# Performance work log

Hardware: AMD Instinct MI355X
Metric: run time of the kernel (lower is better)

The kernel has to match this reference:

```python
import jax, jax.numpy as jnp
import numpy as np

N_NODES = 50000
N_EDGES = 800000
N_GRAPHS = 256
D_IN = 128
D_HID = 128


def setup_inputs() -> dict:
    key = jax.random.key(0)
    ks = jax.random.split(key, 10)
    x = jax.random.normal(ks[0], (N_NODES, D_IN), dtype=jnp.float32)
    edge_index = jax.random.randint(ks[1], (2, N_EDGES), 0, N_NODES, dtype=jnp.int64)
    batch = jnp.sort(jax.random.randint(ks[2], (N_NODES,), 0, N_GRAPHS, dtype=jnp.int64))
    def lin(k, din, dout):
        s = 1.0 / np.sqrt(din)
        return jax.random.uniform(k, (din, dout), jnp.float32, -s, s)
    W1 = lin(ks[3], D_IN, D_HID); b1 = jnp.zeros((D_HID,), jnp.float32)
    W2 = lin(ks[4], D_HID, D_HID); b2 = jnp.zeros((D_HID,), jnp.float32)
    W3 = lin(ks[5], D_HID, D_HID); b3 = jnp.zeros((D_HID,), jnp.float32)
    return {"x": x, "edge_index": edge_index, "batch": batch,
            "W1": W1, "b1": b1, "W2": W2, "b2": b2, "W3": W3, "b3": b3}


def _gcn_norm(edge_index, num_nodes):
    # PyG gcn_norm with add_self_loops=True, edge_weight=1
    loops = jnp.arange(num_nodes, dtype=edge_index.dtype)
    src = jnp.concatenate([edge_index[0], loops])
    dst = jnp.concatenate([edge_index[1], loops])
    ones = jnp.ones(src.shape[0], jnp.float32)
    deg = jax.ops.segment_sum(ones, dst, num_segments=num_nodes)
    dinv = jnp.where(deg > 0, jax.lax.rsqrt(deg), 0.0)
    norm = dinv[src] * dinv[dst]
    return src, dst, norm


def _gcn_conv(x, src, dst, norm, W, b, num_nodes):
    h = x @ W                              # [N, dout] transform first
    msg = h[src] * norm[:, None]           # gather + scale  [E+N, dout]
    agg = jax.ops.segment_sum(msg, dst, num_segments=num_nodes)
    return agg + b


def reference(x, edge_index, batch, W1, b1, W2, b2, W3, b3):
    n = x.shape[0]
    src, dst, norm = _gcn_norm(edge_index, n)
    h = jax.nn.relu(_gcn_conv(x, src, dst, norm, W1, b1, n))
    h = jax.nn.relu(_gcn_conv(h, src, dst, norm, W2, b2, n))
    h = _gcn_conv(h, src, dst, norm, W3, b3, n)
    # global_mean_pool over batch ids
    sums = jax.ops.segment_sum(h, batch, num_segments=N_GRAPHS)
    cnts = jax.ops.segment_sum(jnp.ones((n,), jnp.float32), batch, num_segments=N_GRAPHS)
    return sums / jnp.maximum(cnts, 1.0)[:, None]
```

## Files before the change

### kernel.cpp

```cpp
#include <hip/hip_runtime.h>

#define N_NODES 50000
#define N_PAD   50048
#define N_EDGES 800000
#define N_GRAPHS 256
#define D 128
#define CAP 64
#define GEMM_GRID (N_PAD / 64)

typedef short bf16x8 __attribute__((ext_vector_type(8)));
typedef float f32x4  __attribute__((ext_vector_type(4)));

__device__ inline unsigned short f2bf(float f) {
    unsigned u = __float_as_uint(f);
    u += 0x7FFF + ((u >> 16) & 1);
    return (unsigned short)(u >> 16);
}
__device__ inline float bf2f(unsigned short b) { return __uint_as_float((unsigned)b << 16); }

__global__ __launch_bounds__(256) void k_pack(const float* __restrict__ W1, const float* __restrict__ W2,
                                              const float* __restrict__ W3, unsigned short* __restrict__ Wp) {
    int idx = blockIdx.x * 256 + threadIdx.x;
    if (idx >= 3 * D * D) return;
    int L = idx >> 14, rem = idx & 16383;
    int k = rem >> 7, n = rem & 127;
    const float* W = (L == 0) ? W1 : (L == 1) ? W2 : W3;
    float w = W[k * D + n];
    int kt = k >> 5, kg = (k >> 3) & 3, i = k & 7;
    int nt = n >> 4, ln = kg * 16 + (n & 15);
    size_t dst = (size_t)L * 32768 + ((size_t)(kt * 8 + nt) * 64 + ln) * 8 + i;
    unsigned short hi = f2bf(w);
    Wp[dst]         = hi;
    Wp[dst + 16384] = f2bf(w - bf2f(hi));
}

__global__ __launch_bounds__(256) void k_fill(const int* __restrict__ ei, int* __restrict__ cnt,
                                              int* __restrict__ col) {
    int t = blockIdx.x * 256 + threadIdx.x;
    if (t < N_EDGES / 2) {
        int2 s2 = reinterpret_cast<const int2*>(ei)[t];
        int2 d2 = reinterpret_cast<const int2*>(ei + N_EDGES)[t];
        int p0 = atomicAdd(&cnt[d2.x], 1);
        if (p0 < CAP) col[d2.x * CAP + p0] = s2.x;
        int p1 = atomicAdd(&cnt[d2.y], 1);
        if (p1 < CAP) col[d2.y * CAP + p1] = s2.y;
    }
}


template<bool F32IN>
__global__ __launch_bounds__(256) void k_mfma(const void* __restrict__ Ain,
                                              const unsigned short* __restrict__ Wp,
                                              const int* __restrict__ cnt,
                                              unsigned short* __restrict__ T) {
    int l  = threadIdx.x & 63;
    int wv = threadIdx.x >> 6;
    int row0 = blockIdx.x * 64 + wv * 16;
    int arow = row0 + (l & 15);
    int kchunk = l >> 4;
    const uint4* wp4 = reinterpret_cast<const uint4*>(Wp);

    f32x4 acc[8] = {};
    #pragma unroll
    for (int s = 0; s < 4; ++s) {
        bf16x8 af;
        if (F32IN) {
            float4 a0 = {}, a1 = {};
            if (arow < N_NODES) {
                const float* xr = (const float*)Ain + (size_t)arow * D + s * 32 + kchunk * 8;
                a0 = reinterpret_cast<const float4*>(xr)[0];
                a1 = reinterpret_cast<const float4*>(xr)[1];
            }
            unsigned short h[8] = { f2bf(a0.x), f2bf(a0.y), f2bf(a0.z), f2bf(a0.w),
                                    f2bf(a1.x), f2bf(a1.y), f2bf(a1.z), f2bf(a1.w) };
            __builtin_memcpy(&af, h, 16);
        } else {
            const unsigned short* ar = (const unsigned short*)Ain + (size_t)arow * D;
            uint4 av = reinterpret_cast<const uint4*>(ar)[s * 4 + kchunk];
            __builtin_memcpy(&af, &av, 16);
        }
        #pragma unroll
        for (int nt = 0; nt < 8; ++nt) {
            int f = s * 8 + nt;
            uint4 bh = wp4[f * 64 + l];
            uint4 bl = wp4[f * 64 + l + 2048];
            bf16x8 bhf, blf;
            __builtin_memcpy(&bhf, &bh, 16);
            __builtin_memcpy(&blf, &bl, 16);
            acc[nt] = __builtin_amdgcn_mfma_f32_16x16x32_bf16(af, bhf, acc[nt], 0, 0, 0);
            acc[nt] = __builtin_amdgcn_mfma_f32_16x16x32_bf16(af, blf, acc[nt], 0, 0, 0);
        }
    }

    int rbase = row0 + (l >> 4) * 4;
    int cr = l & 15;
    float sc[4];
    #pragma unroll
    for (int j = 0; j < 4; ++j) {
        int rr = rbase + j;
        sc[j] = (rr < N_NODES) ? rsqrtf((float)cnt[rr] + 1.f) : 0.f;
    }
    #pragma unroll
    for (int nt = 0; nt < 8; ++nt)
        #pragma unroll
        for (int j = 0; j < 4; ++j) {
            int rr = rbase + j;
            if (rr < N_NODES) T[(size_t)rr * D + nt * 16 + cr] = f2bf(acc[nt][j] * sc[j]);
        }
}


template<bool LAST>
__global__ __launch_bounds__(256) void k_agg(const unsigned* __restrict__ Tu, float* __restrict__ AGG,
                                             unsigned* __restrict__ Anext, const float* __restrict__ bias,
                                             const int* __restrict__ cnt, const int* __restrict__ col) {
    int node = blockIdx.x * 4 + (threadIdx.x >> 6);
    int lane = threadIdx.x & 63;
    if (node >= N_NODES) return;

    int len = cnt[node];
    float dd = rsqrtf((float)len + 1.f);
    unsigned ts = Tu[(size_t)node * 64 + lane];
    float2 acc;
    acc.x = __uint_as_float(ts << 16);
    acc.y = __uint_as_float(ts & 0xFFFF0000u);

    const int* crow = col + node * CAP;
    int j = 0;
    for (; j + 4 <= len; j += 4) {
        int4 c = *reinterpret_cast<const int4*>(crow + j);
        unsigned t0 = Tu[(size_t)c.x * 64 + lane];
        unsigned t1 = Tu[(size_t)c.y * 64 + lane];
        unsigned t2 = Tu[(size_t)c.z * 64 + lane];
        unsigned t3 = Tu[(size_t)c.w * 64 + lane];
        acc.x += __uint_as_float(t0 << 16); acc.y += __uint_as_float(t0 & 0xFFFF0000u);
        acc.x += __uint_as_float(t1 << 16); acc.y += __uint_as_float(t1 & 0xFFFF0000u);
        acc.x += __uint_as_float(t2 << 16); acc.y += __uint_as_float(t2 & 0xFFFF0000u);
        acc.x += __uint_as_float(t3 << 16); acc.y += __uint_as_float(t3 & 0xFFFF0000u);
    }
    for (; j < len; ++j) {
        unsigned t0 = Tu[(size_t)crow[j] * 64 + lane];
        acc.x += __uint_as_float(t0 << 16); acc.y += __uint_as_float(t0 & 0xFFFF0000u);
    }

    acc.x *= dd; acc.y *= dd;
    if (!LAST) {
        float rx = fmaxf(acc.x + bias[2 * lane], 0.f);
        float ry = fmaxf(acc.y + bias[2 * lane + 1], 0.f);
        Anext[(size_t)node * 64 + lane] = (unsigned)f2bf(rx) | ((unsigned)f2bf(ry) << 16);
    } else {
        reinterpret_cast<float2*>(AGG)[(size_t)node * 64 + lane] = acc;
    }
}


__global__ __launch_bounds__(128) void k_pool(const float* __restrict__ AGG, const float* __restrict__ b3,
                                              const int* __restrict__ batch, float* __restrict__ out) {
    int g = blockIdx.x;
    int c = threadIdx.x;
    int beg, end;
    { int lo = 0, hi = N_NODES; while (lo < hi) { int m = (lo + hi) >> 1; if (batch[m] < g) lo = m + 1; else hi = m; } beg = lo; }
    { int lo = beg, hi = N_NODES; while (lo < hi) { int m = (lo + hi) >> 1; if (batch[m] < g + 1) lo = m + 1; else hi = m; } end = lo; }
    float acc = 0.f;
    #pragma unroll 4
    for (int i = beg; i < end; ++i) acc += AGG[(size_t)i * D + c];
    int n = end - beg;
    out[g * D + c] = (acc + (float)n * b3[c]) / (float)(n > 0 ? n : 1);
}


static inline size_t align256(size_t x) { return (x + 255) & ~(size_t)255; }

extern "C" void kernel_launch(void* const* d_in, const int* in_sizes, int n_in,
                              void* d_out, int out_size, void* d_ws, size_t ws_size,
                              hipStream_t stream) {
    const float* x    = (const float*)d_in[0];
    const int*  ei    = (const int*)d_in[1];
    const int*  batch = (const int*)d_in[2];
    const float* W1 = (const float*)d_in[3];
    const float* b1 = (const float*)d_in[4];
    const float* W2 = (const float*)d_in[5];
    const float* b2 = (const float*)d_in[6];
    const float* W3 = (const float*)d_in[7];
    const float* b3 = (const float*)d_in[8];
    float* out = (float*)d_out;

    char* ws = (char*)d_ws;
    size_t off = 0;
    auto alloc = [&](size_t bytes) { void* p = ws + off; off = align256(off + bytes); return p; };
    int*   cnt  = (int*)  alloc((size_t)N_NODES * 4);
    int*   col  = (int*)  alloc((size_t)N_NODES * CAP * 4);
    unsigned short* Wp = (unsigned short*)alloc((size_t)3 * 32768 * 2);
    unsigned short* Ab = (unsigned short*)alloc((size_t)N_PAD * D * 2);
    unsigned short* T  = (unsigned short*)alloc((size_t)N_PAD * D * 2);
    float* AGG  = (float*)alloc((size_t)N_NODES * D * 4);
    (void)ws_size; (void)in_sizes; (void)n_in; (void)out_size;

    hipMemsetAsync(cnt, 0, (size_t)N_NODES * 4, stream);

    k_pack<<<(3 * D * D + 255) / 256, 256, 0, stream>>>(W1, W2, W3, Wp);
    k_fill<<<(N_EDGES / 2 + 255) / 256, 256, 0, stream>>>(ei, cnt, col);

    const int agg_grid = (N_NODES + 3) / 4;

    k_mfma<true ><<<GEMM_GRID, 256, 0, stream>>>(x,  Wp,         cnt, T);
    k_agg<false><<<agg_grid, 256, 0, stream>>>((const unsigned*)T, nullptr, (unsigned*)Ab, b1, cnt, col);
    k_mfma<false><<<GEMM_GRID, 256, 0, stream>>>(Ab, Wp + 32768, cnt, T);
    k_agg<false><<<agg_grid, 256, 0, stream>>>((const unsigned*)T, nullptr, (unsigned*)Ab, b2, cnt, col);
    k_mfma<false><<<GEMM_GRID, 256, 0, stream>>>(Ab, Wp + 65536, cnt, T);
    k_agg<true ><<<agg_grid, 256, 0, stream>>>((const unsigned*)T, AGG, nullptr, nullptr, cnt, col);
    k_pool<<<N_GRAPHS, 128, 0, stream>>>(AGG, b3, batch, out);
}
```

Measured before the change: 317.1 us.

## Build adjacency via two-pass bucket partition with 16-bit column indices

Replaces the global-atomic ELL fill with a two-stage build: a block-local histogram partition of edges into 256-node buckets using shared-memory atomics, then a per-bucket kernel that scatters into the per-node column lists with LDS counters. Column indices are stored as 16-bit values, halving adjacency bytes, and the aggregation loop now gathers 8 neighbours per vectorized index load. This is meant to remove contended global atomics and scattered writes during graph construction and to cut index traffic in the three aggregation passes. It adds a kernel launch and a bucket buffer, and it silently drops edges if a bucket holds more than BCAP entries.

```diff
diff --git a/kernel.cpp b/kernel.cpp
--- a/kernel.cpp
+++ b/kernel.cpp
@@ -7,6 +7,11 @@
 #define D 128
 #define CAP 64
 #define GEMM_GRID (N_PAD / 64)
+
+#define NBUCK 196
+#define BCAP  4608
+#define EPB_I4 512
+#define NBLK_A ((N_EDGES / 4 + EPB_I4 - 1) / EPB_I4)
 
 typedef short bf16x8 __attribute__((ext_vector_type(8)));
 typedef float f32x4  __attribute__((ext_vector_type(4)));
@@ -34,17 +39,64 @@
     Wp[dst + 16384] = f2bf(w - bf2f(hi));
 }
 
-__global__ __launch_bounds__(256) void k_fill(const int* __restrict__ ei, int* __restrict__ cnt,
-                                              int* __restrict__ col) {
-    int t = blockIdx.x * 256 + threadIdx.x;
-    if (t < N_EDGES / 2) {
-        int2 s2 = reinterpret_cast<const int2*>(ei)[t];
-        int2 d2 = reinterpret_cast<const int2*>(ei + N_EDGES)[t];
-        int p0 = atomicAdd(&cnt[d2.x], 1);
-        if (p0 < CAP) col[d2.x * CAP + p0] = s2.x;
-        int p1 = atomicAdd(&cnt[d2.y], 1);
-        if (p1 < CAP) col[d2.y * CAP + p1] = s2.y;
-    }
+
+__global__ __launch_bounds__(256) void k_part(const int* __restrict__ ei, int* __restrict__ cursor,
+                                              unsigned* __restrict__ buck) {
+    __shared__ int hist[NBUCK];
+    __shared__ int lbase[NBUCK];
+    for (int i = threadIdx.x; i < NBUCK; i += 256) hist[i] = 0;
+    __syncthreads();
+
+    const int4* s4 = reinterpret_cast<const int4*>(ei);
+    const int4* d4 = reinterpret_cast<const int4*>(ei + N_EDGES);
+    int idx0 = blockIdx.x * EPB_I4 + threadIdx.x;
+    int idx1 = idx0 + 256;
+    bool v0 = idx0 < N_EDGES / 4, v1 = idx1 < N_EDGES / 4;
+    int4 d0 = {}, d1 = {}, s0 = {}, s1 = {};
+    if (v0) {
+        d0 = d4[idx0]; s0 = s4[idx0];
+        atomicAdd(&hist[d0.x >> 8], 1); atomicAdd(&hist[d0.y >> 8], 1);
+        atomicAdd(&hist[d0.z >> 8], 1); atomicAdd(&hist[d0.w >> 8], 1);
+    }
+    if (v1) {
+        d1 = d4[idx1]; s1 = s4[idx1];
+        atomicAdd(&hist[d1.x >> 8], 1); atomicAdd(&hist[d1.y >> 8], 1);
+        atomicAdd(&hist[d1.z >> 8], 1); atomicAdd(&hist[d1.w >> 8], 1);
+    }
+    __syncthreads();
+
+    for (int i = threadIdx.x; i < NBUCK; i += 256)
+        lbase[i] = atomicAdd(&cursor[i], hist[i]);
+    __syncthreads();
+
+    auto put = [&](int d, int s) {
+        int b = d >> 8;
+        int p = atomicAdd(&lbase[b], 1);
+        if (p < BCAP) buck[(size_t)b * BCAP + p] = ((unsigned)(d & 255) << 16) | (unsigned)s;
+    };
+    if (v0) { put(d0.x, s0.x); put(d0.y, s0.y); put(d0.z, s0.z); put(d0.w, s0.w); }
+    if (v1) { put(d1.x, s1.x); put(d1.y, s1.y); put(d1.z, s1.z); put(d1.w, s1.w); }
+}
+
+
+__global__ __launch_bounds__(256) void k_build(const unsigned* __restrict__ buck,
+                                               const int* __restrict__ cursor,
+                                               int* __restrict__ cnt, unsigned short* __restrict__ colu) {
+    __shared__ int lcnt[256];
+    int b = blockIdx.x;
+    lcnt[threadIdx.x] = 0;
+    __syncthreads();
+    int nE = min(cursor[b], BCAP);
+    const unsigned* bb = buck + (size_t)b * BCAP;
+    for (int i = threadIdx.x; i < nE; i += 256) {
+        unsigned v = bb[i];
+        int dl = v >> 16, s = v & 0xFFFF;
+        int p = atomicAdd(&lcnt[dl], 1);
+        if (p < CAP) colu[(size_t)(b * 256 + dl) * CAP + p] = (unsigned short)s;
+    }
+    __syncthreads();
+    int node = b * 256 + threadIdx.x;
+    if (node < N_NODES) cnt[node] = lcnt[threadIdx.x];
 }
 
 
@@ -113,7 +165,7 @@
 template<bool LAST>
 __global__ __launch_bounds__(256) void k_agg(const unsigned* __restrict__ Tu, float* __restrict__ AGG,
                                              unsigned* __restrict__ Anext, const float* __restrict__ bias,
-                                             const int* __restrict__ cnt, const int* __restrict__ col) {
+                                             const int* __restrict__ cnt, const unsigned short* __restrict__ colu) {
     int node = blockIdx.x * 4 + (threadIdx.x >> 6);
     int lane = threadIdx.x & 63;
     if (node >= N_NODES) return;
@@ -125,21 +177,34 @@
     acc.x = __uint_as_float(ts << 16);
     acc.y = __uint_as_float(ts & 0xFFFF0000u);
 
-    const int* crow = col + node * CAP;
+    const unsigned short* crow = colu + (size_t)node * CAP;
     int j = 0;
-    for (; j + 4 <= len; j += 4) {
-        int4 c = *reinterpret_cast<const int4*>(crow + j);
-        unsigned t0 = Tu[(size_t)c.x * 64 + lane];
-        unsigned t1 = Tu[(size_t)c.y * 64 + lane];
-        unsigned t2 = Tu[(size_t)c.z * 64 + lane];
-        unsigned t3 = Tu[(size_t)c.w * 64 + lane];
+    for (; j + 8 <= len; j += 8) {
+        uint4 c = *reinterpret_cast<const uint4*>(crow + j);
+        int s0 = c.x & 0xFFFF, s1 = c.x >> 16;
+        int s2 = c.y & 0xFFFF, s3 = c.y >> 16;
+        int s4 = c.z & 0xFFFF, s5 = c.z >> 16;
+        int s6 = c.w & 0xFFFF, s7 = c.w >> 16;
+        unsigned t0 = Tu[(size_t)s0 * 64 + lane];
+        unsigned t1 = Tu[(size_t)s1 * 64 + lane];
+        unsigned t2 = Tu[(size_t)s2 * 64 + lane];
+        unsigned t3 = Tu[(size_t)s3 * 64 + lane];
+        unsigned t4 = Tu[(size_t)s4 * 64 + lane];
+        unsigned t5 = Tu[(size_t)s5 * 64 + lane];
+        unsigned t6 = Tu[(size_t)s6 * 64 + lane];
+        unsigned t7 = Tu[(size_t)s7 * 64 + lane];
         acc.x += __uint_as_float(t0 << 16); acc.y += __uint_as_float(t0 & 0xFFFF0000u);
         acc.x += __uint_as_float(t1 << 16); acc.y += __uint_as_float(t1 & 0xFFFF0000u);
         acc.x += __uint_as_float(t2 << 16); acc.y += __uint_as_float(t2 & 0xFFFF0000u);
         acc.x += __uint_as_float(t3 << 16); acc.y += __uint_as_float(t3 & 0xFFFF0000u);
+        acc.x += __uint_as_float(t4 << 16); acc.y += __uint_as_float(t4 & 0xFFFF0000u);
+        acc.x += __uint_as_float(t5 << 16); acc.y += __uint_as_float(t5 & 0xFFFF0000u);
+        acc.x += __uint_as_float(t6 << 16); acc.y += __uint_as_float(t6 & 0xFFFF0000u);
+        acc.x += __uint_as_float(t7 << 16); acc.y += __uint_as_float(t7 & 0xFFFF0000u);
     }
     for (; j < len; ++j) {
-        unsigned t0 = Tu[(size_t)crow[j] * 64 + lane];
+        int s = crow[j];
+        unsigned t0 = Tu[(size_t)s * 64 + lane];
         acc.x += __uint_as_float(t0 << 16); acc.y += __uint_as_float(t0 & 0xFFFF0000u);
     }
 
@@ -188,26 +253,29 @@
     char* ws = (char*)d_ws;
     size_t off = 0;
     auto alloc = [&](size_t bytes) { void* p = ws + off; off = align256(off + bytes); return p; };
-    int*   cnt  = (int*)  alloc((size_t)N_NODES * 4);
-    int*   col  = (int*)  alloc((size_t)N_NODES * CAP * 4);
+    int*      cursor = (int*)     alloc((size_t)NBUCK * 4);
+    unsigned* buck   = (unsigned*)alloc((size_t)NBUCK * BCAP * 4);
+    int*      cnt    = (int*)     alloc((size_t)N_NODES * 4);
+    unsigned short* colu = (unsigned short*)alloc((size_t)NBUCK * 256 * CAP * 2);
     unsigned short* Wp = (unsigned short*)alloc((size_t)3 * 32768 * 2);
     unsigned short* Ab = (unsigned short*)alloc((size_t)N_PAD * D * 2);
     unsigned short* T  = (unsigned short*)alloc((size_t)N_PAD * D * 2);
     float* AGG  = (float*)alloc((size_t)N_NODES * D * 4);
     (void)ws_size; (void)in_sizes; (void)n_in; (void)out_size;
 
-    hipMemsetAsync(cnt, 0, (size_t)N_NODES * 4, stream);
-
-    k_pack<<<(3 * D * D + 255) / 256, 256, 0, stream>>>(W1, W2, W3, Wp);
-    k_fill<<<(N_EDGES / 2 + 255) / 256, 256, 0, stream>>>(ei, cnt, col);
+    hipMemsetAsync(cursor, 0, (size_t)NBUCK * 4, stream);
+
+    k_pack <<<(3 * D * D + 255) / 256, 256, 0, stream>>>(W1, W2, W3, Wp);
+    k_part <<<NBLK_A, 256, 0, stream>>>(ei, cursor, buck);
+    k_build<<<NBUCK, 256, 0, stream>>>(buck, cursor, cnt, colu);
 
     const int agg_grid = (N_NODES + 3) / 4;
 
     k_mfma<true ><<<GEMM_GRID, 256, 0, stream>>>(x,  Wp,         cnt, T);
-    k_agg<false><<<agg_grid, 256, 0, stream>>>((const unsigned*)T, nullptr, (unsigned*)Ab, b1, cnt, col);
+    k_agg<false><<<agg_grid, 256, 0, stream>>>((const unsigned*)T, nullptr, (unsigned*)Ab, b1, cnt, colu);
     k_mfma<false><<<GEMM_GRID, 256, 0, stream>>>(Ab, Wp + 32768, cnt, T);
-    k_agg<false><<<agg_grid, 256, 0, stream>>>((const unsigned*)T, nullptr, (unsigned*)Ab, b2, cnt, col);
+    k_agg<false><<<agg_grid, 256, 0, stream>>>((const unsigned*)T, nullptr, (unsigned*)Ab, b2, cnt, colu);
     k_mfma<false><<<GEMM_GRID, 256, 0, stream>>>(Ab, Wp + 65536, cnt, T);
-    k_agg<true ><<<agg_grid, 256, 0, stream>>>((const unsigned*)T, AGG, nullptr, nullptr, cnt, col);
-    k_pool<<<N_GRAPHS, 128, 0, stream>>>(AGG, b3, batch, out);
-}
+    k_agg<true ><<<agg_grid, 256, 0, stream>>>((const unsigned*)T, AGG, nullptr, nullptr, cnt, colu);
+    k_pool <<<N_GRAPHS, 128, 0, stream>>>(AGG, b3, batch, out);
+}
```

After: 293.8 us. 7.4% less time.
